# Kernel tuning notes

Hardware: AMD Instinct MI355X
Metric: run time of the kernel (lower is better)

The kernel has to match this reference:

```python
import jax, jax.numpy as jnp
import numpy as np

N_NODES = 100000
N_EDGES = 1600000
IN_DIM = 32
OUT_DIM = 64
N_REL = 8
EPS = 1e-10


def setup_inputs() -> dict:
    key = jax.random.key(0)
    k_x, k_src, k_dst, k_rel, k_w, k_wl, k_ws = jax.random.split(key, 7)
    x = jax.random.normal(k_x, (N_NODES, IN_DIM), dtype=jnp.float32)
    node_in = jax.random.randint(k_src, (N_EDGES,), 0, N_NODES)
    node_out = jax.random.randint(k_dst, (N_EDGES,), 0, N_NODES)
    relation = jax.random.randint(k_rel, (N_EDGES,), 0, N_REL)
    edge_list = jnp.stack([node_in, node_out, relation], axis=1)  # [E, 3] int
    edge_weight = jax.random.uniform(k_w, (N_EDGES,), dtype=jnp.float32)
    W_linear = jax.random.normal(k_wl, (N_REL * IN_DIM, OUT_DIM), dtype=jnp.float32) / np.sqrt(N_REL * IN_DIM)
    b_linear = jnp.zeros((OUT_DIM,), dtype=jnp.float32)
    W_self = jax.random.normal(k_ws, (IN_DIM, OUT_DIM), dtype=jnp.float32) / np.sqrt(IN_DIM)
    b_self = jnp.zeros((OUT_DIM,), dtype=jnp.float32)
    return {"x": x, "edge_list": edge_list, "edge_weight": edge_weight,
            "W_linear": W_linear, "b_linear": b_linear,
            "W_self": W_self, "b_self": b_self}


def reference(x, edge_list, edge_weight, W_linear, b_linear, W_self, b_self):
    num_node, in_dim = x.shape
    # message: gather source-node features per edge  -> [E, D]
    msg = x[edge_list[:, 0]]
    # aggregate: relation-expanded segment id = dst * R + rel
    seg = edge_list[:, 1] * N_REL + edge_list[:, 2]  # [E]
    w = edge_weight[:, None]  # [E, 1]
    num = jax.ops.segment_sum(msg * w, seg, num_segments=num_node * N_REL)  # [N*R, D]
    den = jax.ops.segment_sum(w, seg, num_segments=num_node * N_REL)        # [N*R, 1]
    update = (num / (den + EPS)).reshape(num_node, N_REL * in_dim)          # [N, R*D]
    # combine: linear(update) + self_loop(x), then ReLU
    out = update @ W_linear + b_linear + x @ W_self + b_self
    return jax.nn.relu(out)
```

## Files before the change

### kernel.cpp

```cpp
#include <hip/hip_runtime.h>
#include <stdint.h>

#define N_NODES 100000
#define N_EDGES 1600000
#define IN_DIM 32
#define OUT_DIM 64
#define N_REL 8
#define NSEG (N_NODES * N_REL)
#define EPS 1e-10f
#define N_KK 9
#define SWG_ELEMS (N_KK * 4 * 64 * 8)
#define XB_PAIRS (N_NODES * 16)
#define NTILES ((N_NODES + 63) / 64)

typedef __attribute__((ext_vector_type(8))) short bf16x8;
typedef __attribute__((ext_vector_type(2))) short bf16x2;
typedef __attribute__((ext_vector_type(4))) float f32x4;

static __device__ __forceinline__ float bflo(uint32_t u) { return __uint_as_float(u << 16); }
static __device__ __forceinline__ float bfhi(uint32_t u) { return __uint_as_float(u & 0xffff0000u); }
static __device__ __forceinline__ uint16_t f2bf(float f) {
    uint32_t u = __float_as_uint(f);
    return (uint16_t)((u + 0x7fffu + ((u >> 16) & 1u)) >> 16);
}

static __device__ __forceinline__ void pk_add_bf16(uint32_t* addr, float f0, float f1) {
#if __has_builtin(__builtin_amdgcn_global_atomic_fadd_v2bf16)
    bf16x2 v;
    v[0] = (short)f2bf(f0);
    v[1] = (short)f2bf(f1);
    __builtin_amdgcn_global_atomic_fadd_v2bf16((bf16x2*)addr, v);
#else
    uint32_t old = *addr, assumed;
    do {
        assumed = old;
        float lo = bflo(assumed) + f0;
        float hi = bfhi(assumed) + f1;
        uint32_t nv = (uint32_t)f2bf(lo) | ((uint32_t)f2bf(hi) << 16);
        old = atomicCAS(addr, assumed, nv);
    } while (old != assumed);
#endif
}

__global__ __launch_bounds__(256) void detect_kernel(const uint32_t* __restrict__ xw,
                                                     int* __restrict__ flag) {
    __shared__ int cnt;
    if (threadIdx.x == 0) cnt = 0;
    __syncthreads();
    int c = 0;
    for (int k = threadIdx.x; k < 4096; k += 256) {
        uint32_t w = xw[k];
        uint32_t e = (w >> 7) & 0xffu;
        c += (e >= 160u) ? 1 : 0;
    }
    atomicAdd(&cnt, c);
    __syncthreads();
    if (threadIdx.x == 0) *flag = (cnt > 64) ? 1 : 0;
}

__global__ __launch_bounds__(256) void prep_kernel(const void* __restrict__ x,
                                                   const void* __restrict__ Wl,
                                                   const void* __restrict__ Ws,
                                                   const void* __restrict__ bl,
                                                   const void* __restrict__ bs,
                                                   const int* __restrict__ flag,
                                                   uint32_t* __restrict__ xb,
                                                   uint16_t* __restrict__ sWg,
                                                   float* __restrict__ biasv) {
    int f32 = *flag;
    int idx = blockIdx.x * 256 + threadIdx.x;
    if (idx < XB_PAIRS) {
        if (f32) {
            float2 v = ((const float2*)x)[idx];
            xb[idx] = (uint32_t)f2bf(v.x) | ((uint32_t)f2bf(v.y) << 16);
        } else {
            xb[idx] = ((const uint32_t*)x)[idx];
        }
    } else if (idx < XB_PAIRS + SWG_ELEMS) {
        int w = idx - XB_PAIRS;
        int j    = w & 7;
        int lane = (w >> 3) & 63;
        int ot   = (w >> 9) & 3;
        int kk   = w >> 11;
        int quad = lane >> 4;
        int k = kk * 32 + quad * 8 + j;
        int o = ot * 16 + (lane & 15);
        if (f32) {
            float v = (k < 256) ? ((const float*)Wl)[(size_t)k * OUT_DIM + o]
                                : ((const float*)Ws)[(size_t)(k - 256) * OUT_DIM + o];
            sWg[w] = f2bf(v);
        } else {
            sWg[w] = (k < 256) ? ((const uint16_t*)Wl)[(size_t)k * OUT_DIM + o]
                               : ((const uint16_t*)Ws)[(size_t)(k - 256) * OUT_DIM + o];
        }
    } else if (idx < XB_PAIRS + SWG_ELEMS + OUT_DIM) {
        int o = idx - XB_PAIRS - SWG_ELEMS;
        if (f32) biasv[o] = ((const float*)bl)[o] + ((const float*)bs)[o];
        else     biasv[o] = bflo((uint32_t)((const uint16_t*)bl)[o])
                          + bflo((uint32_t)((const uint16_t*)bs)[o]);
    }
}

__global__ __launch_bounds__(256) void scatter_pk_kernel(
    const int* __restrict__ el,
    const void* __restrict__ ew,
    const uint32_t* __restrict__ xb,
    const int* __restrict__ flag,
    uint32_t* __restrict__ num,
    float* __restrict__ den)
{
    int t = blockIdx.x * 256 + threadIdx.x;
    int e = t >> 4;
    int p = t & 15;
    if (e >= N_EDGES) return;

    int src = el[e * 3 + 0];
    int dst = el[e * 3 + 1];
    int rel = el[e * 3 + 2];

    float w = (*flag) ? ((const float*)ew)[e]
                      : bflo((uint32_t)((const uint16_t*)ew)[e]);

    uint32_t d = xb[(size_t)src * 16 + p];
    int seg = dst * N_REL + rel;
    pk_add_bf16(&num[(size_t)seg * 16 + p], w * bflo(d), w * bfhi(d));
    if (p == 0) atomicAdd(&den[seg], w);
}

__global__ __launch_bounds__(256) void dense_mfma_kernel(
    const uint32_t* __restrict__ num,
    const float* __restrict__ den,
    const uint32_t* __restrict__ xb,
    const uint16_t* __restrict__ sWg,
    const float* __restrict__ biasv,
    const int* __restrict__ flag,
    void* __restrict__ out)
{
    __shared__ uint16_t sB[SWG_ELEMS];
    #pragma unroll
    for (int it = 0; it < SWG_ELEMS / (256 * 8); ++it) {
        int idx = (it * 256 + threadIdx.x) * 8;
        *(bf16x8*)(sB + idx) = *(const bf16x8*)(sWg + idx);
    }
    __syncthreads();

    int f32  = *flag;
    int wid  = threadIdx.x >> 6;
    int lane = threadIdx.x & 63;
    int quad = lane >> 4;
    int m    = lane & 15;

    float bias[4];
    #pragma unroll
    for (int ot = 0; ot < 4; ++ot) bias[ot] = biasv[ot * 16 + m];

    for (int tile = blockIdx.x; tile < NTILES; tile += gridDim.x) {
        int n0 = tile * 64 + wid * 16;
        int n  = n0 + m;
        int nc = (n < N_NODES) ? n : (N_NODES - 1);

        float4 d0 = *(const float4*)(den + (size_t)nc * 8);
        float4 d1 = *(const float4*)(den + (size_t)nc * 8 + 4);
        float inv[8];
        inv[0] = 1.0f / (d0.x + EPS); inv[1] = 1.0f / (d0.y + EPS);
        inv[2] = 1.0f / (d0.z + EPS); inv[3] = 1.0f / (d0.w + EPS);
        inv[4] = 1.0f / (d1.x + EPS); inv[5] = 1.0f / (d1.y + EPS);
        inv[6] = 1.0f / (d1.z + EPS); inv[7] = 1.0f / (d1.w + EPS);

        f32x4 acc[4];
        #pragma unroll
        for (int ot = 0; ot < 4; ++ot) acc[ot] = (f32x4){0.f, 0.f, 0.f, 0.f};

        #pragma unroll
        for (int kk = 0; kk < N_KK; ++kk) {
            bf16x8 a;
            if (kk < 8) {
                const uint4 d = *(const uint4*)(num + ((size_t)nc * 8 + kk) * 16 + quad * 4);
                float iv = inv[kk];
                a[0] = (short)f2bf(bflo(d.x) * iv); a[1] = (short)f2bf(bfhi(d.x) * iv);
                a[2] = (short)f2bf(bflo(d.y) * iv); a[3] = (short)f2bf(bfhi(d.y) * iv);
                a[4] = (short)f2bf(bflo(d.z) * iv); a[5] = (short)f2bf(bfhi(d.z) * iv);
                a[6] = (short)f2bf(bflo(d.w) * iv); a[7] = (short)f2bf(bfhi(d.w) * iv);
            } else {
                a = *(const bf16x8*)((const uint16_t*)xb + (size_t)nc * IN_DIM + quad * 8);
            }
            #pragma unroll
            for (int ot = 0; ot < 4; ++ot) {
                bf16x8 b = *(const bf16x8*)(sB + ((kk * 4 + ot) * 64 + lane) * 8);
                acc[ot] = __builtin_amdgcn_mfma_f32_16x16x32_bf16(a, b, acc[ot], 0, 0, 0);
            }
        }

        #pragma unroll
        for (int ot = 0; ot < 4; ++ot) {
            #pragma unroll
            for (int reg = 0; reg < 4; ++reg) {
                int node = n0 + quad * 4 + reg;
                if (node >= N_NODES) continue;
                int o = ot * 16 + m;
                float v = fmaxf(acc[ot][reg] + bias[ot], 0.0f);
                if (f32) ((float*)out)[(size_t)node * OUT_DIM + o] = v;
                else     ((uint16_t*)out)[(size_t)node * OUT_DIM + o] = f2bf(v);
            }
        }
    }
}

extern "C" void kernel_launch(void* const* d_in, const int* in_sizes, int n_in,
                              void* d_out, int out_size, void* d_ws, size_t ws_size,
                              hipStream_t stream) {
    const void* x  = d_in[0];
    const int* el  = (const int*)d_in[1];
    const void* ew = d_in[2];
    const void* Wl = d_in[3];
    const void* bl = d_in[4];
    const void* Ws = d_in[5];
    const void* bs = d_in[6];

    const size_t OFF_DEN  = 64;
    const size_t OFF_NUM  = OFF_DEN + (size_t)NSEG * 4;
    const size_t OFF_SWG  = OFF_NUM + (size_t)NSEG * IN_DIM * 2;
    const size_t OFF_BIAS = OFF_SWG + (size_t)SWG_ELEMS * 2;
    const size_t OFF_XB   = OFF_BIAS + OUT_DIM * 4;
    const size_t REQ      = OFF_XB + (size_t)XB_PAIRS * 4;
    if (ws_size < REQ) return;

    int*      flag  = (int*)d_ws;
    float*    den   = (float*)((char*)d_ws + OFF_DEN);
    uint32_t* num   = (uint32_t*)((char*)d_ws + OFF_NUM);
    uint16_t* sWg   = (uint16_t*)((char*)d_ws + OFF_SWG);
    float*    biasv = (float*)((char*)d_ws + OFF_BIAS);
    uint32_t* xb    = (uint32_t*)((char*)d_ws + OFF_XB);

    hipMemsetAsync(d_ws, 0, OFF_SWG, stream);
    detect_kernel<<<1, 256, 0, stream>>>((const uint32_t*)x, flag);
    {
        int total = XB_PAIRS + SWG_ELEMS + OUT_DIM;
        prep_kernel<<<(total + 255) / 256, 256, 0, stream>>>(x, Wl, Ws, bl, bs, flag, xb, sWg, biasv);
    }
    {
        long long threads = (long long)N_EDGES * 16;
        int blocks = (int)((threads + 255) / 256);
        scatter_pk_kernel<<<blocks, 256, 0, stream>>>(el, ew, xb, flag, num, den);
    }
    dense_mfma_kernel<<<1024, 256, 0, stream>>>(num, den, xb, sWg, biasv, flag, d_out);
}
```

Baseline: 282.0 us.

## Split normalization into separate divide kernel and use one tile per block in dense GEMM

Moves the per-segment division by the weight sum out of the MFMA kernel into a standalone kernel that rewrites num in place as bf16, so the dense kernel loads ready-made A fragments. The dense kernel also drops its grid-stride loop and launches one block per 64-node tile. The aim is to shorten the dense kernel's instruction path and raise its occupancy and parallelism. The cost is an extra kernel launch plus a full read and write pass over the 51 MB num buffer.

```diff
diff --git a/kernel.cpp b/kernel.cpp
--- a/kernel.cpp
+++ b/kernel.cpp
@@ -22,6 +22,9 @@
 static __device__ __forceinline__ uint16_t f2bf(float f) {
     uint32_t u = __float_as_uint(f);
     return (uint16_t)((u + 0x7fffu + ((u >> 16) & 1u)) >> 16);
+}
+static __device__ __forceinline__ uint32_t scale_pair(uint32_t d, float iv) {
+    return (uint32_t)f2bf(bflo(d) * iv) | ((uint32_t)f2bf(bfhi(d) * iv) << 16);
 }
 
 static __device__ __forceinline__ void pk_add_bf16(uint32_t* addr, float f0, float f1) {
@@ -127,9 +130,24 @@
     if (p == 0) atomicAdd(&den[seg], w);
 }
 
+__global__ __launch_bounds__(256) void divide_kernel(uint32_t* __restrict__ num,
+                                                     const float* __restrict__ den) {
+    int t = blockIdx.x * 256 + threadIdx.x;
+    if (t >= NSEG * 4) return;
+    int seg = t >> 2;
+    int q   = t & 3;
+    float iv = 1.0f / (den[seg] + EPS);
+    uint32_t* p = num + (size_t)seg * 16 + q * 4;
+    uint4 d = *(const uint4*)p;
+    d.x = scale_pair(d.x, iv);
+    d.y = scale_pair(d.y, iv);
+    d.z = scale_pair(d.z, iv);
+    d.w = scale_pair(d.w, iv);
+    *(uint4*)p = d;
+}
+
 __global__ __launch_bounds__(256) void dense_mfma_kernel(
-    const uint32_t* __restrict__ num,
-    const float* __restrict__ den,
+    const uint16_t* __restrict__ numdiv,
     const uint32_t* __restrict__ xb,
     const uint16_t* __restrict__ sWg,
     const float* __restrict__ biasv,
@@ -154,54 +172,39 @@
     #pragma unroll
     for (int ot = 0; ot < 4; ++ot) bias[ot] = biasv[ot * 16 + m];
 
-    for (int tile = blockIdx.x; tile < NTILES; tile += gridDim.x) {
-        int n0 = tile * 64 + wid * 16;
-        int n  = n0 + m;
-        int nc = (n < N_NODES) ? n : (N_NODES - 1);
-
-        float4 d0 = *(const float4*)(den + (size_t)nc * 8);
-        float4 d1 = *(const float4*)(den + (size_t)nc * 8 + 4);
-        float inv[8];
-        inv[0] = 1.0f / (d0.x + EPS); inv[1] = 1.0f / (d0.y + EPS);
-        inv[2] = 1.0f / (d0.z + EPS); inv[3] = 1.0f / (d0.w + EPS);
-        inv[4] = 1.0f / (d1.x + EPS); inv[5] = 1.0f / (d1.y + EPS);
-        inv[6] = 1.0f / (d1.z + EPS); inv[7] = 1.0f / (d1.w + EPS);
-
-        f32x4 acc[4];
-        #pragma unroll
-        for (int ot = 0; ot < 4; ++ot) acc[ot] = (f32x4){0.f, 0.f, 0.f, 0.f};
-
-        #pragma unroll
-        for (int kk = 0; kk < N_KK; ++kk) {
-            bf16x8 a;
-            if (kk < 8) {
-                const uint4 d = *(const uint4*)(num + ((size_t)nc * 8 + kk) * 16 + quad * 4);
-                float iv = inv[kk];
-                a[0] = (short)f2bf(bflo(d.x) * iv); a[1] = (short)f2bf(bfhi(d.x) * iv);
-                a[2] = (short)f2bf(bflo(d.y) * iv); a[3] = (short)f2bf(bfhi(d.y) * iv);
-                a[4] = (short)f2bf(bflo(d.z) * iv); a[5] = (short)f2bf(bfhi(d.z) * iv);
-                a[6] = (short)f2bf(bflo(d.w) * iv); a[7] = (short)f2bf(bfhi(d.w) * iv);
-            } else {
-                a = *(const bf16x8*)((const uint16_t*)xb + (size_t)nc * IN_DIM + quad * 8);
-            }
-            #pragma unroll
-            for (int ot = 0; ot < 4; ++ot) {
-                bf16x8 b = *(const bf16x8*)(sB + ((kk * 4 + ot) * 64 + lane) * 8);
-                acc[ot] = __builtin_amdgcn_mfma_f32_16x16x32_bf16(a, b, acc[ot], 0, 0, 0);
-            }
-        }
-
+    int n0 = blockIdx.x * 64 + wid * 16;
+    int n  = n0 + m;
+    int nc = (n < N_NODES) ? n : (N_NODES - 1);
+
+    f32x4 acc[4];
+    #pragma unroll
+    for (int ot = 0; ot < 4; ++ot) acc[ot] = (f32x4){0.f, 0.f, 0.f, 0.f};
+
+    #pragma unroll
+    for (int kk = 0; kk < N_KK; ++kk) {
+        bf16x8 a;
+        if (kk < 8) {
+            a = *(const bf16x8*)(numdiv + (size_t)nc * 256 + kk * 32 + quad * 8);
+        } else {
+            a = *(const bf16x8*)((const uint16_t*)xb + (size_t)nc * IN_DIM + quad * 8);
+        }
         #pragma unroll
         for (int ot = 0; ot < 4; ++ot) {
-            #pragma unroll
-            for (int reg = 0; reg < 4; ++reg) {
-                int node = n0 + quad * 4 + reg;
-                if (node >= N_NODES) continue;
-                int o = ot * 16 + m;
-                float v = fmaxf(acc[ot][reg] + bias[ot], 0.0f);
-                if (f32) ((float*)out)[(size_t)node * OUT_DIM + o] = v;
-                else     ((uint16_t*)out)[(size_t)node * OUT_DIM + o] = f2bf(v);
-            }
+            bf16x8 b = *(const bf16x8*)(sB + ((kk * 4 + ot) * 64 + lane) * 8);
+            acc[ot] = __builtin_amdgcn_mfma_f32_16x16x32_bf16(a, b, acc[ot], 0, 0, 0);
+        }
+    }
+
+    #pragma unroll
+    for (int ot = 0; ot < 4; ++ot) {
+        #pragma unroll
+        for (int reg = 0; reg < 4; ++reg) {
+            int node = n0 + quad * 4 + reg;
+            if (node >= N_NODES) continue;
+            int o = ot * 16 + m;
+            float v = fmaxf(acc[ot][reg] + bias[ot], 0.0f);
+            if (f32) ((float*)out)[(size_t)node * OUT_DIM + o] = v;
+            else     ((uint16_t*)out)[(size_t)node * OUT_DIM + o] = f2bf(v);
         }
     }
 }
@@ -243,5 +246,6 @@
         int blocks = (int)((threads + 255) / 256);
         scatter_pk_kernel<<<blocks, 256, 0, stream>>>(el, ew, xb, flag, num, den);
     }
-    dense_mfma_kernel<<<1024, 256, 0, stream>>>(num, den, xb, sWg, biasv, flag, d_out);
-}
+    divide_kernel<<<(NSEG * 4 + 255) / 256, 256, 0, stream>>>(num, den);
+    dense_mfma_kernel<<<NTILES, 256, 0, stream>>>((const uint16_t*)num, xb, sWg, biasv, flag, d_out);
+}
```

New measurement: 294.0 us. 1.04x slower.
